# Optimization experiments

Measured on AMD Instinct MI355X. Metric: run time of the kernel, lower is better.

The kernel has to match this reference:

```python
import jax, jax.numpy as jnp
import numpy as np

B, N, C, H = 2, 2048, 1024, 16
D = C // H  # head dim = 64
SCALE = 1.0 / np.sqrt(D)
BASE = 10000.0  # ntk_factor=1.0 => base unchanged


def setup_inputs() -> dict:
    key = jax.random.key(0)
    k1, k2, k3, k4 = jax.random.split(key, 4)
    x = jax.random.normal(k1, (B, N, C), dtype=jnp.float32)
    Wqkv = jax.random.normal(k2, (C, 3 * C), dtype=jnp.float32) * (1.0 / np.sqrt(C))
    Wout = jax.random.normal(k3, (C, C), dtype=jnp.float32) * (1.0 / np.sqrt(C))
    bout = jax.random.normal(k4, (C,), dtype=jnp.float32) * 0.01
    return {"x": x, "Wqkv": Wqkv, "Wout": Wout, "bout": bout}


def _rope_tables(n, d, dtype):
    inv_freq = 1.0 / (BASE ** (jnp.arange(0, d, 2, dtype=jnp.float32) / d))
    t = jnp.arange(n, dtype=jnp.float32)
    freqs = t[:, None] * inv_freq[None, :]            # [N, D/2]
    cos = jnp.cos(freqs)[None, :, None, :].astype(dtype)  # [1,N,1,D/2]
    sin = jnp.sin(freqs)[None, :, None, :].astype(dtype)
    return cos, sin


def _apply_rope(u, cos, sin):
    # u: [B,N,H,D]; strided-halves RoPE variant (cat, not interleave)
    u1, u2 = u[..., ::2], u[..., 1::2]
    return jnp.concatenate([u1 * cos - u2 * sin, u1 * sin + u2 * cos], axis=-1)


def reference(x, Wqkv, Wout, bout):
    b, n, c = x.shape
    qkv = (x @ Wqkv).reshape(b, n, 3, H, D)
    q, k, v = qkv[:, :, 0], qkv[:, :, 1], qkv[:, :, 2]  # [B,N,H,D]
    cos, sin = _rope_tables(n, D, x.dtype)
    q = _apply_rope(q, cos, sin)
    k = _apply_rope(k, cos, sin)
    scores = jnp.einsum("bqhd,bkhd->bhqk", q, k) * SCALE
    causal = jnp.triu(jnp.ones((n, n), dtype=bool), k=1)
    scores = jnp.where(causal, -jnp.inf, scores)
    attn = jax.nn.softmax(scores, axis=-1)
    out = jnp.einsum("bhqk,bkhd->bqhd", attn, v).reshape(b, n, c)
    return out @ Wout + bout
```

## Files before the change

### kernel.cpp

```cpp
#include <hip/hip_runtime.h>
#include <hip/hip_bf16.h>
#include <math.h>

#define B_ 2
#define N_ 2048
#define C_ 1024
#define H_ 16
#define D_ 64
#define M_ 4096
#define QKV_N 3072
#define SCALE_ 0.125f
#define FIXM 8.0f
#define L2E 1.442695041f

typedef unsigned short u16;
typedef unsigned int u32;
using bf16x8   = __attribute__((ext_vector_type(8))) __bf16;
using ushortx8 = __attribute__((ext_vector_type(8))) unsigned short;
using floatx4  = __attribute__((ext_vector_type(4))) float;
using u32x4    = __attribute__((ext_vector_type(4))) u32;

__device__ __forceinline__ float bf2f(u16 u) {
    union { u32 i; float f; } v; v.i = ((u32)u) << 16; return v.f;
}
__device__ __forceinline__ u16 f2bf(float f) {
    union { float f; u32 i; } v; v.f = f;
    u32 r = (v.i + 0x7fff + ((v.i >> 16) & 1)) >> 16;
    return (u16)r;
}
__device__ __forceinline__ u32 pk2bf(float a, float b) {
    __hip_bfloat162 h = __float22bfloat162_rn(make_float2(a, b));
    union { __hip_bfloat162 h; u32 u; } c; c.h = h; return c.u;
}

__device__ __forceinline__ void gl2lds16(const void* g, void* l) {
    __builtin_amdgcn_global_load_lds(
        (const __attribute__((address_space(1))) unsigned int*)(unsigned long long)g,
        (__attribute__((address_space(3))) unsigned int*)(unsigned long long)l,
        16, 0, 0);
}

__constant__ unsigned char UQI[24] = {7,15,15,14,14,6,13,13,12,12,5,11,11,10,10,4,9,9,8,8,3,2,1,0};
__constant__ unsigned char UT0[24] = {0,0,16,0,15,0,0,14,0,13,0,0,12,0,11,0,0,10,0,9,0,0,0,0};
__constant__ unsigned char UNT[24] = {16,16,16,15,15,14,14,14,13,13,12,12,12,11,11,10,10,10,9,9,8,6,4,2};

__device__ __forceinline__ void do_convtrans(const float* W, u16* Wt, int K, int N,
                                             int nb, int kb, int tid) {
    int n = nb * 256 + tid;
    int k0 = kb * 128;
    #pragma unroll
    for (int kk = 0; kk < 128; kk += 8) {
        ushortx8 v;
        #pragma unroll
        for (int j = 0; j < 8; j++)
            v[j] = f2bf(W[(size_t)(k0 + kk + j) * N + n]);
        *(ushortx8*)(&Wt[(size_t)n * K + k0 + kk]) = v;
    }
}

__global__ __launch_bounds__(256) void prep_kernel(
    const float* __restrict__ x, const float* __restrict__ Wqkv,
    float* __restrict__ cosT, float* __restrict__ sinT,
    u16* __restrict__ xb, u16* __restrict__ Wqkvt)
{
    int bid = blockIdx.x, tid = threadIdx.x;
    if (bid < 2048) {
        int i = bid * 256 + tid;
        const float4* p = (const float4*)x + (size_t)i * 2;
        float4 a = p[0], b = p[1];
        ushortx8 v;
        v[0] = f2bf(a.x); v[1] = f2bf(a.y); v[2] = f2bf(a.z); v[3] = f2bf(a.w);
        v[4] = f2bf(b.x); v[5] = f2bf(b.y); v[6] = f2bf(b.z); v[7] = f2bf(b.w);
        *(ushortx8*)(xb + (size_t)i * 8) = v;
    } else if (bid < 2304) {
        int idx = (bid - 2048) * 256 + tid;
        int n = idx >> 5, i = idx & 31;
        double inv = pow(10000.0, -(double)i / 32.0);
        double f = (double)n * inv;
        cosT[idx] = (float)cos(f);
        sinT[idx] = (float)sin(f);
    } else {
        int u = bid - 2304;
        do_convtrans(Wqkv, Wqkvt, C_, QKV_N, u % 12, u / 12, tid);
    }
}

__global__ __launch_bounds__(256) void gemm128(
    const u16* __restrict__ A, const u16* __restrict__ Bt,
    void* __restrict__ Cm, const float* __restrict__ bias, int fp32out,
    u16* __restrict__ Vt,
    int M, int N, int K)
{
    __shared__ u16 As[128 * 32];
    __shared__ u16 Bs[128 * 32];
    const int t = threadIdx.x;
    const int w = t >> 6, lane = t & 63;
    const int quad = lane >> 4, cc = lane & 15;
    const int m0 = blockIdx.y * 128, n0 = blockIdx.x * 128;
    const int wm = (w >> 1) * 64, wn = (w & 1) * 64;

    floatx4 acc[4][4];
    floatx4 zero = {0.f, 0.f, 0.f, 0.f};
    #pragma unroll
    for (int i = 0; i < 4; i++)
        #pragma unroll
        for (int j = 0; j < 4; j++) acc[i][j] = zero;

    const int srow = lane >> 2, skof = (lane & 3) * 8;

    for (int k0 = 0; k0 < K; k0 += 32) {
        __syncthreads();
        #pragma unroll
        for (int c = 0; c < 2; c++) {
            int chunk = w * 2 + c;
            int row = chunk * 16 + srow;
            gl2lds16(A  + (size_t)(m0 + row) * K + k0 + skof, (char*)As + chunk * 1024);
            gl2lds16(Bt + (size_t)(n0 + row) * K + k0 + skof, (char*)Bs + chunk * 1024);
        }
        __syncthreads();

        bf16x8 af[4], bf[4];
        #pragma unroll
        for (int i = 0; i < 4; i++)
            af[i] = *(const bf16x8*)(&As[(wm + i * 16 + cc) * 32 + quad * 8]);
        #pragma unroll
        for (int j = 0; j < 4; j++)
            bf[j] = *(const bf16x8*)(&Bs[(wn + j * 16 + cc) * 32 + quad * 8]);
        #pragma unroll
        for (int i = 0; i < 4; i++)
            #pragma unroll
            for (int j = 0; j < 4; j++)
                acc[i][j] = __builtin_amdgcn_mfma_f32_16x16x32_bf16(af[i], bf[j], acc[i][j], 0, 0, 0);
    }

    if (Vt && n0 >= 2048) {
        #pragma unroll
        for (int i = 0; i < 4; i++)
            #pragma unroll
            for (int j = 0; j < 4; j++)
                #pragma unroll
                for (int r = 0; r < 4; r++) {
                    int row = m0 + wm + i * 16 + quad * 4 + r;
                    int col2 = n0 + wn + j * 16 + cc - 2048;
                    int h = col2 >> 6, d = col2 & 63;
                    int b = row >> 11, n = row & 2047;
                    int nl = n & 63;
                    size_t idx = (size_t)(b * H_ + h) * (N_ * D_) + (size_t)(n >> 6) * 4096
                               + (size_t)(((nl >> 5) * 4 + ((nl >> 2) & 3)) * 64 + d) * 8
                               + ((nl >> 4) & 1) * 4 + (nl & 3);
                    Vt[idx] = f2bf(acc[i][j][r]);
                }
        return;
    }

    #pragma unroll
    for (int i = 0; i < 4; i++)
        #pragma unroll
        for (int j = 0; j < 4; j++)
            #pragma unroll
            for (int r = 0; r < 4; r++) {
                int row = m0 + wm + i * 16 + quad * 4 + r;
                int col = n0 + wn + j * 16 + cc;
                float v = acc[i][j][r];
                if (fp32out) ((float*)Cm)[(size_t)row * N + col] = v + bias[col];
                else         ((u16*)Cm)[(size_t)row * N + col] = f2bf(v);
            }
}

__global__ void rope_kernel(const u16* __restrict__ qkv,
                            const float* __restrict__ cosT, const float* __restrict__ sinT,
                            u16* __restrict__ Qh, u16* __restrict__ Kh)
{
    int idx = blockIdx.x * 256 + threadIdx.x;
    if (idx >= B_ * N_ * H_ * 32) return;
    int i = idx & 31;
    int h = (idx >> 5) & (H_ - 1);
    int n = (idx >> 9) & (N_ - 1);
    int b = idx >> 20;
    size_t m = (size_t)b * N_ + n;
    const u16* row = qkv + m * QKV_N;
    float cs = cosT[n * 32 + i], sn = sinT[n * 32 + i];

    float q1 = bf2f(row[h * 64 + 2 * i]),      q2 = bf2f(row[h * 64 + 2 * i + 1]);
    float k1 = bf2f(row[C_ + h * 64 + 2 * i]), k2 = bf2f(row[C_ + h * 64 + 2 * i + 1]);
    size_t obase = ((size_t)(b * H_ + h) * N_ + n) * D_;
    Qh[obase + i]      = f2bf((q1 * cs - q2 * sn) * SCALE_);
    Qh[obase + 32 + i] = f2bf((q1 * sn + q2 * cs) * SCALE_);
    Kh[obase + i]      = f2bf(k1 * cs - k2 * sn);
    Kh[obase + 32 + i] = f2bf(k1 * sn + k2 * cs);
}

__global__ __launch_bounds__(256, 3) void attn_kernel(
    const u16* __restrict__ Qh, const u16* __restrict__ Kh,
    const u16* __restrict__ Vt, u16* __restrict__ Ao,
    u16* __restrict__ Opart, float* __restrict__ lpart)
{
    __shared__ u16 Ks[2][64 * 64];
    __shared__ u16 Vs[2][64 * 64];

    const int t = threadIdx.x;
    const int wave = t >> 6, lane = t & 63;
    const int quad = lane >> 4, cc = lane & 15;

    int id = blockIdx.x + 24 * blockIdx.y;
    int e8 = id & 7, s = id >> 3;
    const int u = s % 24;
    const int bh = e8 + 8 * (s / 24);

    const int qi = UQI[u], tile0 = UT0[u], ntl = UNT[u];
    const int qb0 = qi * 128;
    const size_t hb = (size_t)bh * N_ * D_;
    const int qlocal = wave * 16 + cc;

    const int r8 = lane >> 3, sl = lane & 7;
    const int swz = (sl ^ r8) * 8;

    auto STAGE = [&](int kb, int c) {
        #pragma unroll
        for (int i = 0; i < 2; i++) {
            int shot = wave * 2 + i;
            int row = shot * 8 + r8;
            gl2lds16(Kh + hb + (size_t)(kb + row) * 64 + swz, (char*)Ks[c] + shot * 1024);
            gl2lds16(Vt + hb + (size_t)kb * 64 + (size_t)row * 64 + swz, (char*)Vs[c] + shot * 1024);
        }
    };

    bf16x8 qf[2][2];
    #pragma unroll
    for (int qt = 0; qt < 2; qt++) {
        const u16* qrow = Qh + hb + (size_t)(qb0 + qt * 64 + wave * 16 + cc) * D_;
        qf[qt][0] = *(const bf16x8*)(qrow + quad * 8);
        qf[qt][1] = *(const bf16x8*)(qrow + 32 + quad * 8);
    }

    floatx4 zero = {0.f, 0.f, 0.f, 0.f};
    floatx4 Oacc[2][4];
    float lsum[2] = {0.f, 0.f};
    #pragma unroll
    for (int qt = 0; qt < 2; qt++)
        #pragma unroll
        for (int j = 0; j < 4; j++) Oacc[qt][j] = zero;

    STAGE(tile0 * 64, 0);
    __syncthreads();

    for (int ti = 0; ti < ntl; ti++) {
        const int kb = (tile0 + ti) * 64;
        const int c = ti & 1;
        if (ti + 1 < ntl) STAGE(kb + 64, c ^ 1);
        const bool act0 = (kb <= qb0);

        bf16x8 kf[4][2];
        #pragma unroll
        for (int nt = 0; nt < 4; nt++)
            #pragma unroll
            for (int sfr = 0; sfr < 2; sfr++)
                kf[nt][sfr] = *(const bf16x8*)(
                    &Ks[c][(nt * 16 + cc) * 64 + (((sfr * 4 + quad) ^ (cc & 7)) * 8)]);

        u32 pa[2][4][2];

        {
            floatx4 S[4];
            __builtin_amdgcn_s_setprio(1);
            #pragma unroll
            for (int nt = 0; nt < 4; nt++) {
                floatx4 a = zero;
                a = __builtin_amdgcn_mfma_f32_16x16x32_bf16(kf[nt][0], qf[1][0], a, 0, 0, 0);
                a = __builtin_amdgcn_mfma_f32_16x16x32_bf16(kf[nt][1], qf[1][1], a, 0, 0, 0);
                S[nt] = a;
            }
            __builtin_amdgcn_s_setprio(0);
            const bool diag = (kb == qb0 + 64);
            #pragma unroll
            for (int nt = 0; nt < 4; nt++) {
                float p[4];
                #pragma unroll
                for (int r = 0; r < 4; r++) {
                    int key_l = nt * 16 + quad * 4 + r;
                    float ex = exp2f(fmaf(S[nt][r], L2E, -FIXM * L2E));
                    p[r] = (diag && (key_l > qlocal)) ? 0.0f : ex;
                    lsum[1] += p[r];
                }
                pa[1][nt][0] = pk2bf(p[0], p[1]);
                pa[1][nt][1] = pk2bf(p[2], p[3]);
            }
        }

        if (act0) {
            floatx4 S0[4];
            __builtin_amdgcn_s_setprio(1);
            #pragma unroll
            for (int nt = 0; nt < 4; nt++) {
                floatx4 a = zero;
                a = __builtin_amdgcn_mfma_f32_16x16x32_bf16(kf[nt][0], qf[0][0], a, 0, 0, 0);
                a = __builtin_amdgcn_mfma_f32_16x16x32_bf16(kf[nt][1], qf[0][1], a, 0, 0, 0);
                S0[nt] = a;
            }
            __builtin_amdgcn_s_setprio(0);
            const bool diag = (kb == qb0);
            #pragma unroll
            for (int nt = 0; nt < 4; nt++) {
                float p[4];
                #pragma unroll
                for (int r = 0; r < 4; r++) {
                    int key_l = nt * 16 + quad * 4 + r;
                    float ex = exp2f(fmaf(S0[nt][r], L2E, -FIXM * L2E));
                    p[r] = (diag && (key_l > qlocal)) ? 0.0f : ex;
                    lsum[0] += p[r];
                }
                pa[0][nt][0] = pk2bf(p[0], p[1]);
                pa[0][nt][1] = pk2bf(p[2], p[3]);
            }
        }

        __builtin_amdgcn_s_setprio(1);
        #pragma unroll
        for (int g = 0; g < 2; g++) {
            u32x4 aa1 = {pa[1][2 * g][0], pa[1][2 * g][1], pa[1][2 * g + 1][0], pa[1][2 * g + 1][1]};
            bf16x8 A1 = __builtin_bit_cast(bf16x8, aa1);
            bf16x8 A0;
            if (act0) {
                u32x4 aa0 = {pa[0][2 * g][0], pa[0][2 * g][1], pa[0][2 * g + 1][0], pa[0][2 * g + 1][1]};
                A0 = __builtin_bit_cast(bf16x8, aa0);
            }
            #pragma unroll
            for (int j = 0; j < 4; j++) {
                int vrow = (g * 4 + quad) * 8 + j * 2 + (cc >> 3);
                bf16x8 v8 = *(const bf16x8*)(
                    &Vs[c][vrow * 64 + (((cc & 7) ^ (vrow & 7)) * 8)]);
                Oacc[1][j] = __builtin_amdgcn_mfma_f32_16x16x32_bf16(A1, v8, Oacc[1][j], 0, 0, 0);
                if (act0)
                    Oacc[0][j] = __builtin_amdgcn_mfma_f32_16x16x32_bf16(A0, v8, Oacc[0][j], 0, 0, 0);
            }
        }
        __builtin_amdgcn_s_setprio(0);

        __syncthreads();
    }

    const bool partial = (qi >= 8);
    const int cid = (tile0 > 0) ? 1 : 0;
    const int slot = ((bh * 8 + (qi - 8)) * 2 + cid);
    const int b = bh >> 4, h = bh & (H_ - 1);

    #pragma unroll
    for (int qt = 0; qt < 2; qt++) {
        float lf = lsum[qt];
        lf += __shfl_xor(lf, 16, 64);
        lf += __shfl_xor(lf, 32, 64);
        if (!partial) {
            #pragma unroll
            for (int r = 0; r < 4; r++) {
                float l_r = __shfl(lf, quad * 4 + r, 64);
                float inv = 1.0f / l_r;
                int n = qb0 + qt * 64 + wave * 16 + quad * 4 + r;
                #pragma unroll
                for (int j = 0; j < 4; j++)
                    Ao[((size_t)b * N_ + n) * C_ + h * D_ + j * 16 + cc] = f2bf(Oacc[qt][j][r] * inv);
            }
        } else {
            #pragma unroll
            for (int r = 0; r < 4; r++) {
                int lrow = qt * 64 + wave * 16 + quad * 4 + r;
                u16* Ob = Opart + (size_t)slot * (128 * 64) + (size_t)lrow * 64;
                #pragma unroll
                for (int j = 0; j < 4; j++)
                    Ob[j * 16 + cc] = f2bf(Oacc[qt][j][r]);
            }
            if (lane < 16)
                lpart[slot * 128 + qt * 64 + wave * 16 + cc] = lf;
        }
    }
}

__global__ __launch_bounds__(256) void attn_combine(
    const u16* __restrict__ Opart, const float* __restrict__ lpart,
    u16* __restrict__ Ao, const float* __restrict__ Wout, u16* __restrict__ Woutt)
{
    if (blockIdx.x >= 2048) {
        int u = blockIdx.x - 2048;
        do_convtrans(Wout, Woutt, C_, C_, u % 4, u / 4, threadIdx.x);
        return;
    }
    int g = blockIdx.x * 256 + threadIdx.x;
    int f4 = g & 15;
    int row = (g >> 4) & 127;
    int qz = (g >> 11) & 7;
    int bh = g >> 14;
    int s0 = (bh * 8 + qz) * 2;
    const u16* O0 = Opart + (size_t)s0 * (128 * 64) + (size_t)row * 64 + f4 * 4;
    const u16* O1 = O0 + 128 * 64;
    float l = lpart[s0 * 128 + row] + lpart[(s0 + 1) * 128 + row];
    float inv = 1.0f / l;
    ushort4 a = *(const ushort4*)O0, c = *(const ushort4*)O1;
    int b = bh >> 4, h = bh & (H_ - 1);
    int n = (qz + 8) * 128 + row;
    u16* d = Ao + ((size_t)b * N_ + n) * C_ + h * D_ + f4 * 4;
    d[0] = f2bf((bf2f(a.x) + bf2f(c.x)) * inv);
    d[1] = f2bf((bf2f(a.y) + bf2f(c.y)) * inv);
    d[2] = f2bf((bf2f(a.z) + bf2f(c.z)) * inv);
    d[3] = f2bf((bf2f(a.w) + bf2f(c.w)) * inv);
}

extern "C" void kernel_launch(void* const* d_in, const int* in_sizes, int n_in,
                              void* d_out, int out_size, void* d_ws, size_t ws_size,
                              hipStream_t stream)
{
    const float* x    = (const float*)d_in[0];
    const float* Wqkv = (const float*)d_in[1];
    const float* Wout = (const float*)d_in[2];
    const float* bout = (const float*)d_in[3];

    char* p = (char*)d_ws;
    u16* qkv = (u16*)p; p += (size_t)M_ * QKV_N * 2;
    u16* Qh  = (u16*)p; p += (size_t)B_ * H_ * N_ * D_ * 2;
    u16* Kh  = (u16*)p; p += (size_t)B_ * H_ * N_ * D_ * 2;
    u16* Vt  = (u16*)p; p += (size_t)B_ * H_ * N_ * D_ * 2;
    u16* Ao  = (u16*)p; p += (size_t)M_ * C_ * 2;
    float* cosT = (float*)p; p += (size_t)N_ * 32 * 4;
    float* sinT = (float*)p; p += (size_t)N_ * 32 * 4;

    u16* xb    = Ao;
    u16* Wqkvt = Qh;
    u16* Woutt = qkv;
    u16* Opart = (u16*)((char*)qkv + ((size_t)2 << 20));
    float* lpart = (float*)((char*)qkv + ((size_t)21 << 20));

    hipLaunchKernelGGL(prep_kernel, dim3(2400), dim3(256), 0, stream,
                       x, Wqkv, cosT, sinT, xb, Wqkvt);
    hipLaunchKernelGGL(gemm128, dim3(QKV_N / 128, M_ / 128), dim3(256), 0, stream,
                       xb, Wqkvt, qkv, (const float*)nullptr, 0, Vt, M_, QKV_N, C_);
    hipLaunchKernelGGL(rope_kernel, dim3((B_ * N_ * H_ * 32) / 256), dim3(256), 0, stream,
                       qkv, cosT, sinT, Qh, Kh);
    hipLaunchKernelGGL(attn_kernel, dim3(24, B_ * H_), dim3(256), 0, stream,
                       Qh, Kh, Vt, Ao, Opart, lpart);
    hipLaunchKernelGGL(attn_combine, dim3(2048 + 32), dim3(256), 0, stream,
                       Opart, lpart, Ao, Wout, Woutt);
    hipLaunchKernelGGL(gemm128, dim3(C_ / 128, M_ / 128), dim3(256), 0, stream,
                       Ao, Woutt, d_out, bout, 1, (u16*)nullptr, M_, C_, C_);
}
```

Measured before the change: 223.3 us.

## Split causal attention into finer KV chunks and compute row sums via MFMA

Reworks the causal attention work split from 24 to 40 work units per head, each covering at most 8 KV tiles, so query blocks from index 4 upward are split into 2-4 partial chunks. The combine kernel now sums a variable number of partials per row. The scalar per-lane row-sum accumulation and its cross-lane shuffles are replaced by an extra MFMA against a ones vector, which yields row sums directly in the accumulator layout. The launch-bounds occupancy hint rises from 3 to 4 blocks. This is meant to give better load balance and more parallelism, at the cost of more partial-output traffic, a heavier combine step and extra MFMA work.

New measurement: 255.6 us. 14.4% more time.

```diff
diff --git a/kernel.cpp b/kernel.cpp
--- a/kernel.cpp
+++ b/kernel.cpp
@@ -40,9 +40,12 @@
         16, 0, 0);
 }
 
-__constant__ unsigned char UQI[24] = {7,15,15,14,14,6,13,13,12,12,5,11,11,10,10,4,9,9,8,8,3,2,1,0};
-__constant__ unsigned char UT0[24] = {0,0,16,0,15,0,0,14,0,13,0,0,12,0,11,0,0,10,0,9,0,0,0,0};
-__constant__ unsigned char UNT[24] = {16,16,16,15,15,14,14,14,13,13,12,12,12,11,11,10,10,10,9,9,8,6,4,2};
+__constant__ unsigned char UQI[40] = {3,7,7,10,11,11,11,14,14,15,15,15,15,6,6,9,9,10,10,12,12,13,13,13,13,14,14,2,5,5,8,8,8,9,12,12,4,4,1,0};
+__constant__ unsigned char UT0[40] = {0,0,8,0,0,8,16,0,8,0,8,16,24,0,7,0,7,8,15,0,7,0,7,14,21,16,23,0,0,6,0,6,12,14,14,20,0,5,0,0};
+__constant__ unsigned char UNT[40] = {8,8,8,8,8,8,8,8,8,8,8,8,8,7,7,7,7,7,7,7,7,7,7,7,7,7,7,6,6,6,6,6,6,6,6,6,5,5,4,2};
+__constant__ unsigned char UCID[40] = {0,0,1,0,0,1,2,0,1,0,1,2,3,0,1,0,1,1,2,0,1,0,1,2,3,2,3,0,0,1,0,1,2,2,2,3,0,1,0,0};
+__constant__ unsigned char CCNT[12] = {2,2,2,2,3,3,3,3,4,4,4,4};
+__constant__ unsigned char SOFF[12] = {0,2,4,6,8,11,14,17,20,24,28,32};
 
 __device__ __forceinline__ void do_convtrans(const float* W, u16* Wt, int K, int N,
                                              int nb, int kb, int tid) {
@@ -190,7 +193,7 @@
     Kh[obase + 32 + i] = f2bf(k1 * sn + k2 * cs);
 }
 
-__global__ __launch_bounds__(256, 3) void attn_kernel(
+__global__ __launch_bounds__(256, 4) void attn_kernel(
     const u16* __restrict__ Qh, const u16* __restrict__ Kh,
     const u16* __restrict__ Vt, u16* __restrict__ Ao,
     u16* __restrict__ Opart, float* __restrict__ lpart)
@@ -202,12 +205,12 @@
     const int wave = t >> 6, lane = t & 63;
     const int quad = lane >> 4, cc = lane & 15;
 
-    int id = blockIdx.x + 24 * blockIdx.y;
+    int id = blockIdx.x + 40 * blockIdx.y;
     int e8 = id & 7, s = id >> 3;
-    const int u = s % 24;
-    const int bh = e8 + 8 * (s / 24);
-
-    const int qi = UQI[u], tile0 = UT0[u], ntl = UNT[u];
+    const int u = s % 40;
+    const int bh = e8 + 8 * (s / 40);
+
+    const int qi = UQI[u], tile0 = UT0[u], ntl = UNT[u], cid = UCID[u];
     const int qb0 = qi * 128;
     const size_t hb = (size_t)bh * N_ * D_;
     const int qlocal = wave * 16 + cc;
@@ -233,13 +236,18 @@
         qf[qt][1] = *(const bf16x8*)(qrow + 32 + quad * 8);
     }
 
+    const u32x4 onesw = {0x3F803F80u, 0x3F803F80u, 0x3F803F80u, 0x3F803F80u};
+    const bf16x8 ones8 = __builtin_bit_cast(bf16x8, onesw);
+
     floatx4 zero = {0.f, 0.f, 0.f, 0.f};
     floatx4 Oacc[2][4];
-    float lsum[2] = {0.f, 0.f};
-    #pragma unroll
-    for (int qt = 0; qt < 2; qt++)
+    floatx4 Osum[2];
+    #pragma unroll
+    for (int qt = 0; qt < 2; qt++) {
+        Osum[qt] = zero;
         #pragma unroll
         for (int j = 0; j < 4; j++) Oacc[qt][j] = zero;
+    }
 
     STAGE(tile0 * 64, 0);
     __syncthreads();
@@ -280,7 +288,6 @@
                     int key_l = nt * 16 + quad * 4 + r;
                     float ex = exp2f(fmaf(S[nt][r], L2E, -FIXM * L2E));
                     p[r] = (diag && (key_l > qlocal)) ? 0.0f : ex;
-                    lsum[1] += p[r];
                 }
                 pa[1][nt][0] = pk2bf(p[0], p[1]);
                 pa[1][nt][1] = pk2bf(p[2], p[3]);
@@ -307,7 +314,6 @@
                     int key_l = nt * 16 + quad * 4 + r;
                     float ex = exp2f(fmaf(S0[nt][r], L2E, -FIXM * L2E));
                     p[r] = (diag && (key_l > qlocal)) ? 0.0f : ex;
-                    lsum[0] += p[r];
                 }
                 pa[0][nt][0] = pk2bf(p[0], p[1]);
                 pa[0][nt][1] = pk2bf(p[2], p[3]);
@@ -333,27 +339,25 @@
                 if (act0)
                     Oacc[0][j] = __builtin_amdgcn_mfma_f32_16x16x32_bf16(A0, v8, Oacc[0][j], 0, 0, 0);
             }
+            Osum[1] = __builtin_amdgcn_mfma_f32_16x16x32_bf16(A1, ones8, Osum[1], 0, 0, 0);
+            if (act0)
+                Osum[0] = __builtin_amdgcn_mfma_f32_16x16x32_bf16(A0, ones8, Osum[0], 0, 0, 0);
         }
         __builtin_amdgcn_s_setprio(0);
 
         __syncthreads();
     }
 
-    const bool partial = (qi >= 8);
-    const int cid = (tile0 > 0) ? 1 : 0;
-    const int slot = ((bh * 8 + (qi - 8)) * 2 + cid);
+    const bool partial = (qi >= 4);
+    const int slot = bh * 36 + SOFF[qi - 4] + cid;
     const int b = bh >> 4, h = bh & (H_ - 1);
 
     #pragma unroll
     for (int qt = 0; qt < 2; qt++) {
-        float lf = lsum[qt];
-        lf += __shfl_xor(lf, 16, 64);
-        lf += __shfl_xor(lf, 32, 64);
         if (!partial) {
             #pragma unroll
             for (int r = 0; r < 4; r++) {
-                float l_r = __shfl(lf, quad * 4 + r, 64);
-                float inv = 1.0f / l_r;
+                float inv = 1.0f / Osum[qt][r];
                 int n = qb0 + qt * 64 + wave * 16 + quad * 4 + r;
                 #pragma unroll
                 for (int j = 0; j < 4; j++)
@@ -368,8 +372,11 @@
                 for (int j = 0; j < 4; j++)
                     Ob[j * 16 + cc] = f2bf(Oacc[qt][j][r]);
             }
-            if (lane < 16)
-                lpart[slot * 128 + qt * 64 + wave * 16 + cc] = lf;
+            if (cc == 0) {
+                #pragma unroll
+                for (int r = 0; r < 4; r++)
+                    lpart[slot * 128 + qt * 64 + wave * 16 + quad * 4 + r] = Osum[qt][r];
+            }
         }
     }
 }
@@ -378,29 +385,33 @@
     const u16* __restrict__ Opart, const float* __restrict__ lpart,
     u16* __restrict__ Ao, const float* __restrict__ Wout, u16* __restrict__ Woutt)
 {
-    if (blockIdx.x >= 2048) {
-        int u = blockIdx.x - 2048;
+    if (blockIdx.x >= 3072) {
+        int u = blockIdx.x - 3072;
         do_convtrans(Wout, Woutt, C_, C_, u % 4, u / 4, threadIdx.x);
         return;
     }
     int g = blockIdx.x * 256 + threadIdx.x;
     int f4 = g & 15;
     int row = (g >> 4) & 127;
-    int qz = (g >> 11) & 7;
-    int bh = g >> 14;
-    int s0 = (bh * 8 + qz) * 2;
-    const u16* O0 = Opart + (size_t)s0 * (128 * 64) + (size_t)row * 64 + f4 * 4;
-    const u16* O1 = O0 + 128 * 64;
-    float l = lpart[s0 * 128 + row] + lpart[(s0 + 1) * 128 + row];
+    int v = g >> 11;
+    int qz = v % 12, bh = v / 12;
+    int cnt = CCNT[qz];
+    int s0 = bh * 36 + SOFF[qz];
+    float l = 0.f, a0 = 0.f, a1 = 0.f, a2 = 0.f, a3 = 0.f;
+    for (int c2 = 0; c2 < cnt; c2++) {
+        l += lpart[(s0 + c2) * 128 + row];
+        const u16* O = Opart + (size_t)(s0 + c2) * (128 * 64) + (size_t)row * 64 + f4 * 4;
+        ushort4 a = *(const ushort4*)O;
+        a0 += bf2f(a.x); a1 += bf2f(a.y); a2 += bf2f(a.z); a3 += bf2f(a.w);
+    }
     float inv = 1.0f / l;
-    ushort4 a = *(const ushort4*)O0, c = *(const ushort4*)O1;
     int b = bh >> 4, h = bh & (H_ - 1);
-    int n = (qz + 8) * 128 + row;
+    int n = (qz + 4) * 128 + row;
     u16* d = Ao + ((size_t)b * N_ + n) * C_ + h * D_ + f4 * 4;
-    d[0] = f2bf((bf2f(a.x) + bf2f(c.x)) * inv);
-    d[1] = f2bf((bf2f(a.y) + bf2f(c.y)) * inv);
-    d[2] = f2bf((bf2f(a.z) + bf2f(c.z)) * inv);
-    d[3] = f2bf((bf2f(a.w) + bf2f(c.w)) * inv);
+    d[0] = f2bf(a0 * inv);
+    d[1] = f2bf(a1 * inv);
+    d[2] = f2bf(a2 * inv);
+    d[3] = f2bf(a3 * inv);
 }
 
 extern "C" void kernel_launch(void* const* d_in, const int* in_sizes, int n_in,
@@ -433,9 +444,9 @@
                        xb, Wqkvt, qkv, (const float*)nullptr, 0, Vt, M_, QKV_N, C_);
     hipLaunchKernelGGL(rope_kernel, dim3((B_ * N_ * H_ * 32) / 256), dim3(256), 0, stream,
                        qkv, cosT, sinT, Qh, Kh);
-    hipLaunchKernelGGL(attn_kernel, dim3(24, B_ * H_), dim3(256), 0, stream,
+    hipLaunchKernelGGL(attn_kernel, dim3(40, B_ * H_), dim3(256), 0, stream,
                        Qh, Kh, Vt, Ao, Opart, lpart);
-    hipLaunchKernelGGL(attn_combine, dim3(2048 + 32), dim3(256), 0, stream,
+    hipLaunchKernelGGL(attn_combine, dim3(3072 + 32), dim3(256), 0, stream,
                        Opart, lpart, Ao, Wout, Woutt);
     hipLaunchKernelGGL(gemm128, dim3(C_ / 128, M_ / 128), dim3(256), 0, stream,
                        Ao, Woutt, d_out, bout, 1, (u16*)nullptr, M_, C_, C_);
```
